# Performance work log

Measured on AMD Instinct MI355X. Metric: run time of the kernel, lower is better.

## Reference

```python
import jax, jax.numpy as jnp
import numpy as np

EPS = 1e-4  # matches init_kwargs eps


def setup_inputs() -> dict:
    key = jax.random.key(0)
    k1, k2, k3 = jax.random.split(key, 3)
    B, C, T = 64, 256, 2048
    x = jax.random.normal(k1, (B, C, T), dtype=jnp.float32)
    # per-timestep BatchNorm affine params: [T, C]
    gamma = 1.0 + 0.1 * jax.random.normal(k2, (T, C), dtype=jnp.float32)
    beta = 0.01 * jax.random.normal(k3, (T, C), dtype=jnp.float32)
    return {"x": x, "gamma": gamma, "beta": beta}


def reference(x, gamma, beta):
    # BNTTv1 (training mode): every timestep's BatchNorm1d sees the FULL [B, C, T]
    # tensor, so the batch statistics (per-channel mean/var over B and T) are
    # identical across timesteps. Only the affine (gamma_t, beta_t) differs, and
    # the module keeps just slice t of layer t's output. Equivalent fused form:
    mean = jnp.mean(x, axis=(0, 2), keepdims=True)            # [1, C, 1]
    var = jnp.mean((x - mean) ** 2, axis=(0, 2), keepdims=True)  # biased var
    norm = (x - mean) * jax.lax.rsqrt(var + EPS)              # [B, C, T]
    # gamma/beta: [T, C] -> broadcast as [1, C, T]
    out = norm * gamma.T[None, :, :] + beta.T[None, :, :]
    return out
```

## Files before the change

kernel.cpp:

```cpp
#include <hip/hip_runtime.h>

#define B_ 64
#define C_ 256
#define T_ 2048
#define EPS_ 1e-4f
#define NPC ((float)(B_ * T_))

#define SPLITS 8
#define BPB (B_ / SPLITS)
#define T4 (T_ / 4)

#define CTILE 16
#define T4TILE 16
#define BCHUNK 32

typedef float f4 __attribute__((ext_vector_type(4)));

__global__ __launch_bounds__(256) void bntt_stats(const float* __restrict__ x,
                                                  float* __restrict__ partials) {
    const int c   = blockIdx.x & (C_ - 1);
    const int s   = blockIdx.x >> 8;
    const int tid = threadIdx.x;

    float sum = 0.0f, sumsq = 0.0f;
    const int b0 = s * BPB;
    #pragma unroll
    for (int b = 0; b < BPB; ++b) {
        const f4* p = (const f4*)(x + (size_t)(b0 + b) * (C_ * T_) + (size_t)c * T_);
        #pragma unroll
        for (int i = 0; i < T4 / 256; ++i) {
            f4 v = p[tid + i * 256];
            sum   += v.x + v.y + v.z + v.w;
            sumsq += v.x * v.x + v.y * v.y + v.z * v.z + v.w * v.w;
        }
    }
    #pragma unroll
    for (int off = 32; off > 0; off >>= 1) {
        sum   += __shfl_down(sum, off);
        sumsq += __shfl_down(sumsq, off);
    }
    __shared__ float ls[4], lss[4];
    const int wave = tid >> 6, lane = tid & 63;
    if (lane == 0) { ls[wave] = sum; lss[wave] = sumsq; }
    __syncthreads();
    if (tid == 0) {
        partials[s * C_ + c]               = ls[0] + ls[1] + ls[2] + ls[3];
        partials[SPLITS * C_ + s * C_ + c] = lss[0] + lss[1] + lss[2] + lss[3];
    }
}

__global__ __launch_bounds__(256) void bntt_norm(const float* __restrict__ x,
                                                 const float* __restrict__ gamma,
                                                 const float* __restrict__ beta,
                                                 const float* __restrict__ partials,
                                                 float* __restrict__ out) {
    __shared__ float sg[64][17];
    __shared__ float sb[64][17];
    __shared__ float smean[CTILE], sistd[CTILE];

    const int tid    = threadIdx.x;
    const int tile   = blockIdx.x & 511;
    const int c0     = (tile >> 5) * CTILE;
    const int t4base = (tile & 31) * T4TILE;
    const int b0     = (blockIdx.x >> 9) * BCHUNK;

    if (tid < CTILE) {
        const int c = c0 + tid;
        float S = 0.0f, SS = 0.0f;
        #pragma unroll
        for (int s = 0; s < SPLITS; ++s) {
            S  += partials[s * C_ + c];
            SS += partials[SPLITS * C_ + s * C_ + c];
        }
        const float mean = S / NPC;
        smean[tid] = mean;
        sistd[tid] = rsqrtf(SS / NPC - mean * mean + EPS_);
    }

    {
        const int cl = tid & 15;
        const int tl0 = tid >> 4;
        const int tbase = t4base * 4;
        #pragma unroll
        for (int it = 0; it < 4; ++it) {
            const int tl = tl0 + it * 16;
            const size_t gi = (size_t)(tbase + tl) * C_ + (c0 + cl);
            sg[tl][cl] = gamma[gi];
            sb[tl][cl] = beta[gi];
        }
    }
    __syncthreads();

    const int t4i = tid & 15;
    const int ci  = tid >> 4;
    const float mean = smean[ci];
    const float istd = sistd[ci];
    f4 sc, sh;
    #pragma unroll
    for (int j = 0; j < 4; ++j) {
        const int tl = t4i * 4 + j;
        const float s1 = sg[tl][ci] * istd;
        ((float*)&sc)[j] = s1;
        ((float*)&sh)[j] = fmaf(-mean, s1, sb[tl][ci]);
    }

    size_t idx = ((size_t)b0 * C_ + (c0 + ci)) * T4 + (t4base + t4i);
    const size_t step = (size_t)C_ * T4;
    #pragma unroll 4
    for (int b = 0; b < BCHUNK; ++b) {
        f4 xv = ((const f4*)x)[idx];
        f4 o;
        o.x = fmaf(xv.x, sc.x, sh.x);
        o.y = fmaf(xv.y, sc.y, sh.y);
        o.z = fmaf(xv.z, sc.z, sh.z);
        o.w = fmaf(xv.w, sc.w, sh.w);
        __builtin_nontemporal_store(o, &((f4*)out)[idx]);
        idx += step;
    }
}

extern "C" void kernel_launch(void* const* d_in, const int* in_sizes, int n_in,
                              void* d_out, int out_size, void* d_ws, size_t ws_size,
                              hipStream_t stream) {
    const float* x     = (const float*)d_in[0];
    const float* gamma = (const float*)d_in[1];
    const float* beta  = (const float*)d_in[2];
    float* out = (float*)d_out;
    float* partials = (float*)d_ws;

    bntt_stats<<<C_ * SPLITS, 256, 0, stream>>>(x, partials);

    const int ngrid = (C_ / CTILE) * (T4 / T4TILE) * (B_ / BCHUNK);
    bntt_norm<<<ngrid, 256, 0, stream>>>(x, gamma, beta, partials, out);
}
```

Measured before the change: 251.6 us.

## Restructure stats pass into per-batch channel-group blocks with 64-way partials

The stats kernel now assigns each block one batch row and a group of 8 contiguous channels, so it reads a contiguous 64KB slab and reduces per-channel through shared memory. It writes 64 per-batch partials per channel instead of 8 splits. The norm kernel reduces these 64 partials cooperatively with 128 threads, and its unroll factor rises to 8. A fallback path keeps the old kernels for when the workspace is too small, at the cost of a slightly heavier partial reduction in every norm block.

Measured after the change: 256.4 us. No clear change (+1.9%).

```diff
diff --git a/kernel.cpp b/kernel.cpp
--- a/kernel.cpp
+++ b/kernel.cpp
@@ -6,9 +6,8 @@
 #define EPS_ 1e-4f
 #define NPC ((float)(B_ * T_))
 
-#define SPLITS 8
-#define BPB (B_ / SPLITS)
 #define T4 (T_ / 4)
+#define CG_ 8
 
 #define CTILE 16
 #define T4TILE 16
@@ -18,34 +17,47 @@
 
 __global__ __launch_bounds__(256) void bntt_stats(const float* __restrict__ x,
                                                   float* __restrict__ partials) {
-    const int c   = blockIdx.x & (C_ - 1);
-    const int s   = blockIdx.x >> 8;
+    const int bid = blockIdx.x;
+    const int b   = bid >> 5;
+    const int cg  = bid & 31;
     const int tid = threadIdx.x;
-
-    float sum = 0.0f, sumsq = 0.0f;
-    const int b0 = s * BPB;
-    #pragma unroll
-    for (int b = 0; b < BPB; ++b) {
-        const f4* p = (const f4*)(x + (size_t)(b0 + b) * (C_ * T_) + (size_t)c * T_);
-        #pragma unroll
-        for (int i = 0; i < T4 / 256; ++i) {
-            f4 v = p[tid + i * 256];
-            sum   += v.x + v.y + v.z + v.w;
-            sumsq += v.x * v.x + v.y * v.y + v.z * v.z + v.w * v.w;
-        }
-    }
-    #pragma unroll
-    for (int off = 32; off > 0; off >>= 1) {
-        sum   += __shfl_down(sum, off);
-        sumsq += __shfl_down(sumsq, off);
-    }
-    __shared__ float ls[4], lss[4];
-    const int wave = tid >> 6, lane = tid & 63;
-    if (lane == 0) { ls[wave] = sum; lss[wave] = sumsq; }
-    __syncthreads();
-    if (tid == 0) {
-        partials[s * C_ + c]               = ls[0] + ls[1] + ls[2] + ls[3];
-        partials[SPLITS * C_ + s * C_ + c] = lss[0] + lss[1] + lss[2] + lss[3];
+    const f4* p = (const f4*)(x + ((size_t)b * C_ + (size_t)cg * CG_) * T_);
+
+    float sum[CG_], ssq[CG_];
+    #pragma unroll
+    for (int k = 0; k < CG_; ++k) { sum[k] = 0.0f; ssq[k] = 0.0f; }
+
+    #pragma unroll
+    for (int i = 0; i < 16; ++i) {
+        f4 v = p[tid + i * 256];
+        const int k = i >> 1;
+        sum[k] += v.x + v.y + v.z + v.w;
+        ssq[k] += v.x * v.x + v.y * v.y + v.z * v.z + v.w * v.w;
+    }
+
+    __shared__ float ls[CG_][256];
+    __shared__ float lq[CG_][256];
+    #pragma unroll
+    for (int k = 0; k < CG_; ++k) { ls[k][tid] = sum[k]; lq[k][tid] = ssq[k]; }
+    __syncthreads();
+
+    const int k = tid >> 5;
+    const int j = tid & 31;
+    float S = 0.0f, SS = 0.0f;
+    #pragma unroll
+    for (int m = 0; m < 8; ++m) {
+        S  += ls[k][j + m * 32];
+        SS += lq[k][j + m * 32];
+    }
+    #pragma unroll
+    for (int off = 16; off > 0; off >>= 1) {
+        S  += __shfl_down(S, off);
+        SS += __shfl_down(SS, off);
+    }
+    if (j == 0) {
+        const size_t c = (size_t)cg * CG_ + k;
+        partials[(size_t)b * C_ + c]                      = S;
+        partials[(size_t)B_ * C_ + (size_t)b * C_ + c]    = SS;
     }
 }
 
@@ -56,6 +68,7 @@
                                                  float* __restrict__ out) {
     __shared__ float sg[64][17];
     __shared__ float sb[64][17];
+    __shared__ float psum[CTILE][8], psq[CTILE][8];
     __shared__ float smean[CTILE], sistd[CTILE];
 
     const int tid    = threadIdx.x;
@@ -64,21 +77,8 @@
     const int t4base = (tile & 31) * T4TILE;
     const int b0     = (blockIdx.x >> 9) * BCHUNK;
 
-    if (tid < CTILE) {
-        const int c = c0 + tid;
-        float S = 0.0f, SS = 0.0f;
-        #pragma unroll
-        for (int s = 0; s < SPLITS; ++s) {
-            S  += partials[s * C_ + c];
-            SS += partials[SPLITS * C_ + s * C_ + c];
-        }
-        const float mean = S / NPC;
-        smean[tid] = mean;
-        sistd[tid] = rsqrtf(SS / NPC - mean * mean + EPS_);
-    }
-
     {
-        const int cl = tid & 15;
+        const int cl  = tid & 15;
         const int tl0 = tid >> 4;
         const int tbase = t4base * 4;
         #pragma unroll
@@ -89,6 +89,31 @@
             sb[tl][cl] = beta[gi];
         }
     }
+
+    if (tid < 128) {
+        const int cl = tid & 15;
+        const int h  = tid >> 4;
+        const int c  = c0 + cl;
+        float S = 0.0f, SS = 0.0f;
+        #pragma unroll
+        for (int m = 0; m < 8; ++m) {
+            const size_t b = (size_t)(h * 8 + m);
+            S  += partials[b * C_ + c];
+            SS += partials[(size_t)B_ * C_ + b * C_ + c];
+        }
+        psum[cl][h] = S;
+        psq[cl][h]  = SS;
+    }
+    __syncthreads();
+
+    if (tid < CTILE) {
+        float S = 0.0f, SS = 0.0f;
+        #pragma unroll
+        for (int h = 0; h < 8; ++h) { S += psum[tid][h]; SS += psq[tid][h]; }
+        const float mean = S / NPC;
+        smean[tid] = mean;
+        sistd[tid] = rsqrtf(SS / NPC - mean * mean + EPS_);
+    }
     __syncthreads();
 
     const int t4i = tid & 15;
@@ -106,7 +131,7 @@
 
     size_t idx = ((size_t)b0 * C_ + (c0 + ci)) * T4 + (t4base + t4i);
     const size_t step = (size_t)C_ * T4;
-    #pragma unroll 4
+    #pragma unroll 8
     for (int b = 0; b < BCHUNK; ++b) {
         f4 xv = ((const f4*)x)[idx];
         f4 o;
@@ -119,6 +144,84 @@
     }
 }
 
+#define SPLITS 8
+#define BPB (B_ / SPLITS)
+__global__ __launch_bounds__(256) void bntt_stats_fb(const float* __restrict__ x,
+                                                     float* __restrict__ partials) {
+    const int c   = blockIdx.x & (C_ - 1);
+    const int s   = blockIdx.x >> 8;
+    const int tid = threadIdx.x;
+    float sum = 0.0f, sumsq = 0.0f;
+    const int b0 = s * BPB;
+    #pragma unroll
+    for (int b = 0; b < BPB; ++b) {
+        const f4* p = (const f4*)(x + (size_t)(b0 + b) * (C_ * T_) + (size_t)c * T_);
+        #pragma unroll
+        for (int i = 0; i < T4 / 256; ++i) {
+            f4 v = p[tid + i * 256];
+            sum   += v.x + v.y + v.z + v.w;
+            sumsq += v.x * v.x + v.y * v.y + v.z * v.z + v.w * v.w;
+        }
+    }
+    #pragma unroll
+    for (int off = 32; off > 0; off >>= 1) {
+        sum   += __shfl_down(sum, off);
+        sumsq += __shfl_down(sumsq, off);
+    }
+    __shared__ float ls2[4], lss2[4];
+    const int wave = tid >> 6, lane = tid & 63;
+    if (lane == 0) { ls2[wave] = sum; lss2[wave] = sumsq; }
+    __syncthreads();
+    if (tid == 0) {
+        partials[s * C_ + c]               = ls2[0] + ls2[1] + ls2[2] + ls2[3];
+        partials[SPLITS * C_ + s * C_ + c] = lss2[0] + lss2[1] + lss2[2] + lss2[3];
+    }
+}
+
+__global__ __launch_bounds__(256) void bntt_norm_fb(const float* __restrict__ x,
+                                                    const float* __restrict__ gamma,
+                                                    const float* __restrict__ beta,
+                                                    const float* __restrict__ partials,
+                                                    float* __restrict__ out) {
+    const int p   = (blockIdx.x & 511) * 256 + threadIdx.x;
+    const int c   = p >> 9;
+    const int t4  = p & (T4 - 1);
+    const int t   = t4 * 4;
+    const int b0  = (blockIdx.x >> 9) * BCHUNK;
+
+    float S = 0.0f, SS = 0.0f;
+    #pragma unroll
+    for (int s = 0; s < SPLITS; ++s) {
+        S  += partials[s * C_ + c];
+        SS += partials[SPLITS * C_ + s * C_ + c];
+    }
+    const float mean = S / NPC;
+    const float istd = rsqrtf(SS / NPC - mean * mean + EPS_);
+
+    f4 sc, sh;
+    #pragma unroll
+    for (int j = 0; j < 4; ++j) {
+        float g  = gamma[(size_t)(t + j) * C_ + c];
+        float bb = beta [(size_t)(t + j) * C_ + c];
+        float s1 = g * istd;
+        ((float*)&sc)[j] = s1;
+        ((float*)&sh)[j] = fmaf(-mean, s1, bb);
+    }
+    size_t idx = (size_t)(b0 * C_ + c) * T4 + t4;
+    const size_t step = (size_t)C_ * T4;
+    #pragma unroll 8
+    for (int b = 0; b < BCHUNK; ++b) {
+        f4 xv = ((const f4*)x)[idx];
+        f4 o;
+        o.x = fmaf(xv.x, sc.x, sh.x);
+        o.y = fmaf(xv.y, sc.y, sh.y);
+        o.z = fmaf(xv.z, sc.z, sh.z);
+        o.w = fmaf(xv.w, sc.w, sh.w);
+        __builtin_nontemporal_store(o, &((f4*)out)[idx]);
+        idx += step;
+    }
+}
+
 extern "C" void kernel_launch(void* const* d_in, const int* in_sizes, int n_in,
                               void* d_out, int out_size, void* d_ws, size_t ws_size,
                               hipStream_t stream) {
@@ -128,8 +231,13 @@
     float* out = (float*)d_out;
     float* partials = (float*)d_ws;
 
-    bntt_stats<<<C_ * SPLITS, 256, 0, stream>>>(x, partials);
-
     const int ngrid = (C_ / CTILE) * (T4 / T4TILE) * (B_ / BCHUNK);
-    bntt_norm<<<ngrid, 256, 0, stream>>>(x, gamma, beta, partials, out);
-}
+
+    if (ws_size >= (size_t)2 * B_ * C_ * sizeof(float)) {
+        bntt_stats<<<B_ * (C_ / CG_), 256, 0, stream>>>(x, partials);
+        bntt_norm<<<ngrid, 256, 0, stream>>>(x, gamma, beta, partials, out);
+    } else {
+        bntt_stats_fb<<<C_ * SPLITS, 256, 0, stream>>>(x, partials);
+        bntt_norm_fb<<<ngrid, 256, 0, stream>>>(x, gamma, beta, partials, out);
+    }
+}
```
